# Kernel tuning notes

Measured on AMD Instinct MI355X. Metric: run time of the kernel, lower is better.

## Reference

```python
import jax, jax.numpy as jnp
import numpy as np

B, H, W, C = 4, 64, 64, 256
CQ = C // 8


def setup_inputs() -> dict:
    key = jax.random.key(0)
    ks = jax.random.split(key, 5)
    scale = 0.02
    inputs = jax.random.normal(ks[0], (B, H, W, C), dtype=jnp.float32)
    wq = jax.random.normal(ks[1], (C, CQ), dtype=jnp.float32) * scale
    bq = jnp.zeros((CQ,), dtype=jnp.float32)
    wk = jax.random.normal(ks[2], (C, CQ), dtype=jnp.float32) * scale
    bk = jnp.zeros((CQ,), dtype=jnp.float32)
    wv = jax.random.normal(ks[3], (C, C), dtype=jnp.float32) * scale
    bv = jnp.zeros((C,), dtype=jnp.float32)
    gamma = jax.random.normal(ks[4], (), dtype=jnp.float32)
    return {"inputs": inputs, "wq": wq, "bq": bq, "wk": wk, "bk": bk,
            "wv": wv, "bv": bv, "gamma": gamma}


def reference(inputs, wq, bq, wk, bk, wv, bv, gamma):
    b, h, w, c = inputs.shape
    n = h * w
    x = inputs.reshape(b, n, c)  # [B, N, C]
    # 1x1 convs == per-pixel linear projections
    q = x @ wq + bq              # [B, N, Cq]
    k = x @ wk + bk              # [B, N, Cq]
    v = x @ wv + bv              # [B, N, C]
    # energy = Q K^T (no sqrt scaling, as in the original)
    energy = jnp.einsum('bnd,bmd->bnm', q, k)      # [B, N, N]
    attention = jax.nn.softmax(energy, axis=-1)    # softmax over keys
    # x_out = V^T @ attention^T -> per query: sum_m attn[n,m] * v[m]
    x_out = jnp.einsum('bnm,bmc->bnc', attention, v)  # [B, N, C]
    x_out = x_out.reshape(b, h, w, c)
    return gamma * x_out + inputs
```

## Files before the change

kernel.cpp:

```cpp
#include <hip/hip_runtime.h>
#include <hip/hip_bf16.h>

typedef __attribute__((ext_vector_type(8))) short bf16x8;
typedef __attribute__((ext_vector_type(4))) float f32x4;
typedef __attribute__((ext_vector_type(16))) float f32x16;
typedef __attribute__((ext_vector_type(4))) int int4v;

#define NB 4
#define NN 4096
#define NC 256
#define NSPLIT 4
#define KEYS_PER_SPLIT 1024
#define KT_ITERS 16
#define LOG2E 1.4426950408889634f

__device__ __forceinline__ unsigned short f2bf(float f) {
    unsigned u = __builtin_bit_cast(unsigned, f);
    u += 0x7fffu + ((u >> 16) & 1u);
    return (unsigned short)(u >> 16);
}
__device__ __forceinline__ float bf2f(unsigned short u) {
    unsigned v = ((unsigned)u) << 16;
    return __builtin_bit_cast(float, v);
}
__device__ __forceinline__ void load_lds16(const void* g, void* l) {
    __builtin_amdgcn_global_load_lds(
        (const __attribute__((address_space(1))) void*)g,
        (__attribute__((address_space(3))) void*)l, 16, 0, 0);
}
__device__ __forceinline__ unsigned cvtpk(float lo, float hi) {
    unsigned d;
    asm("v_cvt_pk_bf16_f32 %0, %1, %2" : "=v"(d) : "v"(lo), "v"(hi));
    return d;
}
__device__ __forceinline__ void pl32swap(unsigned &a, unsigned &b) {
    asm volatile("v_permlane32_swap_b32 %0, %1" : "+v"(a), "+v"(b));
}
__device__ __forceinline__ float fexp2(float x) {
    float r;
    asm("v_exp_f32 %0, %1" : "=v"(r) : "v"(x));
    return r;
}

__global__ __launch_bounds__(256) void wt_kernel(
    const float* __restrict__ wq, const float* __restrict__ wk,
    const float* __restrict__ wv, unsigned short* __restrict__ wt)
{
    const int c = blockIdx.x;
    const int k = threadIdx.x;
    float v;
    if (c < 32)      v = wq[k * 32 + c];
    else if (c < 64) v = wk[k * 32 + (c - 32)] * LOG2E;
    else             v = wv[k * 256 + (c - 64)];
    wt[c * 256 + k] = f2bf(v);
}

__global__ __launch_bounds__(256) void proj_kernel(
    const float* __restrict__ x,
    const unsigned short* __restrict__ wt,
    const float* __restrict__ bq, const float* __restrict__ bk,
    const float* __restrict__ bv,
    unsigned short* __restrict__ q_ws,
    unsigned short* __restrict__ k_ws,
    unsigned short* __restrict__ vt_ws)
{
    const int lane = threadIdx.x & 63;
    const int w    = threadIdx.x >> 6;
    const int l15  = lane & 15, hh = lane >> 4;
    const int m0   = blockIdx.x * 16;
    const int ct0  = w * 5;

    f32x4 acc[5];
    #pragma unroll
    for (int i = 0; i < 5; ++i) acc[i] = f32x4{0.f, 0.f, 0.f, 0.f};

    const float* xrow = x + (size_t)(m0 + l15) * 256 + hh * 8;
    #pragma unroll
    for (int ks = 0; ks < 8; ++ks) {
        float4 xa = ((const float4*)(xrow + ks * 32))[0];
        float4 xb = ((const float4*)(xrow + ks * 32))[1];
        bf16x8 afrag;
        afrag[0] = (short)f2bf(xa.x); afrag[1] = (short)f2bf(xa.y);
        afrag[2] = (short)f2bf(xa.z); afrag[3] = (short)f2bf(xa.w);
        afrag[4] = (short)f2bf(xb.x); afrag[5] = (short)f2bf(xb.y);
        afrag[6] = (short)f2bf(xb.z); afrag[7] = (short)f2bf(xb.w);
        #pragma unroll
        for (int c = 0; c < 5; ++c) {
            bf16x8 bfrag = *(const bf16x8*)(wt + (size_t)((ct0 + c) * 16 + l15) * 256 + ks * 32 + hh * 8);
            acc[c] = __builtin_amdgcn_mfma_f32_16x16x32_bf16(afrag, bfrag, acc[c], 0, 0, 0);
        }
    }

    const int b    = m0 >> 12;
    const int nloc = m0 & 4095;
    #pragma unroll
    for (int c = 0; c < 5; ++c) {
        const int ct = ct0 + c;
        const int c0 = ct * 16;
        float bias;
        if (c0 < 32)      bias = bq[c0 + l15];
        else if (c0 < 64) bias = bk[c0 - 32 + l15] * LOG2E;
        else              bias = bv[c0 - 64 + l15];
        if (c0 < 64) {
            unsigned short* dst = (c0 < 32) ? q_ws : k_ws;
            const int cc = (c0 < 32) ? c0 : (c0 - 32);
            #pragma unroll
            for (int i = 0; i < 4; ++i)
                dst[(size_t)(m0 + hh * 4 + i) * 32 + cc + l15] = f2bf(acc[c][i] + bias);
        } else {
            const int cc = c0 - 64 + l15;
            #pragma unroll
            for (int i = 0; i < 4; i += 2) {
                unsigned lo = f2bf(acc[c][i]     + bias);
                unsigned hi = f2bf(acc[c][i + 1] + bias);
                *(unsigned*)(vt_ws + ((size_t)b * 256 + cc) * 4096 + nloc + hh * 4 + i)
                    = lo | (hi << 16);
            }
        }
    }
}

__global__ __launch_bounds__(256, 4) void attn_kernel(
    const unsigned short* __restrict__ q_ws,
    const unsigned short* __restrict__ k_ws,
    const unsigned short* __restrict__ vt_ws,
    unsigned short* __restrict__ opart,
    float* __restrict__ lpart)
{
    __shared__ unsigned short vt_lds[256 * 64];

    const int lane = threadIdx.x & 63;
    const int wid  = threadIdx.x >> 6;
    const int l31  = lane & 31;
    const int hi   = lane >> 5;
    const int wr   = wid >> 1;
    const int wc   = wid & 1;

    const int xcd   = blockIdx.x & 7;
    const int j     = blockIdx.x >> 3;
    const int combo = xcd * 2 + (j >> 6);
    const int qtile = j & 63;
    const int split = combo >> 2;
    const int b     = combo & 3;
    const int q0    = qtile * 64;
    const int key0  = split * KEYS_PER_SPLIT;

    bf16x8 aq[2];
    #pragma unroll
    for (int cs = 0; cs < 2; ++cs)
        aq[cs] = *(const bf16x8*)(q_ws +
            (size_t)(b * 4096 + q0 + wr * 32 + l31) * 32 + cs * 16 + hi * 8);

    f32x16 acc[4];
    #pragma unroll
    for (int ct = 0; ct < 4; ++ct)
        #pragma unroll
        for (int r = 0; r < 16; ++r) acc[ct][r] = 0.f;
    float lsum = 0.f;

    const unsigned short* vt_base = vt_ws + (size_t)b * 256 * 4096;
    const unsigned short* k_base  = k_ws + (size_t)b * 4096 * 32;

    for (int kt = 0; kt < KT_ITERS; ++kt) {
        const int kb = key0 + kt * 64;
        __syncthreads();

        #pragma unroll
        for (int e = 0; e < 8; ++e) {
            int idx  = e * 256 + threadIdx.x;
            int c    = idx >> 3;
            int slot = idx & 7;
            const unsigned short* src = vt_base + (size_t)c * 4096 + kb + ((slot ^ (c & 7)) << 3);
            load_lds16(src, (char*)vt_lds + idx * 16);
        }

        unsigned pa[4][4];
        #pragma unroll
        for (int ktile = 0; ktile < 2; ++ktile) {
            bf16x8 ak0 = *(const bf16x8*)(k_base +
                (size_t)(kb + ktile * 32 + l31) * 32 + hi * 8);
            bf16x8 ak1 = *(const bf16x8*)(k_base +
                (size_t)(kb + ktile * 32 + l31) * 32 + 16 + hi * 8);
            f32x16 e0;
            #pragma unroll
            for (int r = 0; r < 16; ++r) e0[r] = 0.f;
            e0 = __builtin_amdgcn_mfma_f32_32x32x16_bf16(ak0, aq[0], e0, 0, 0, 0);
            e0 = __builtin_amdgcn_mfma_f32_32x32x16_bf16(ak1, aq[1], e0, 0, 0, 0);

            float s = 0.f;
            #pragma unroll
            for (int h = 0; h < 2; ++h) {
                float p0 = fexp2(e0[h*8+0]), p1 = fexp2(e0[h*8+1]);
                float p2 = fexp2(e0[h*8+2]), p3 = fexp2(e0[h*8+3]);
                float p4 = fexp2(e0[h*8+4]), p5 = fexp2(e0[h*8+5]);
                float p6 = fexp2(e0[h*8+6]), p7 = fexp2(e0[h*8+7]);
                s += ((p0 + p1) + (p2 + p3)) + ((p4 + p5) + (p6 + p7));
                unsigned d0 = cvtpk(p0, p1);
                unsigned d1 = cvtpk(p2, p3);
                unsigned d2 = cvtpk(p4, p5);
                unsigned d3 = cvtpk(p6, p7);
                pl32swap(d0, d2);
                pl32swap(d1, d3);
                const int ks = ktile * 2 + h;
                pa[ks][0] = d0; pa[ks][1] = d1;
                pa[ks][2] = d2; pa[ks][3] = d3;
            }
            lsum += s;
        }
        __syncthreads();

        __builtin_amdgcn_s_setprio(1);
        #pragma unroll
        for (int ks = 0; ks < 4; ++ks) {
            union { unsigned u[4]; bf16x8 v; } cvt;
            cvt.u[0] = pa[ks][0]; cvt.u[1] = pa[ks][1];
            cvt.u[2] = pa[ks][2]; cvt.u[3] = pa[ks][3];
            #pragma unroll
            for (int ct = 0; ct < 4; ++ct) {
                int c = wc * 128 + ct * 32 + l31;
                int chunk = ks * 2 + hi;
                bf16x8 bvf = *(const bf16x8*)((char*)vt_lds + c * 128 + ((chunk ^ (c & 7)) << 4));
                acc[ct] = __builtin_amdgcn_mfma_f32_32x32x16_bf16(cvt.v, bvf, acc[ct], 0, 0, 0);
            }
        }
        __builtin_amdgcn_s_setprio(0);
    }

    lsum += __shfl_xor(lsum, 32);

    const size_t rowb = (size_t)(split * 4 + b) * 4096 + q0 + wr * 32;
    if (wc == 0 && hi == 0)
        lpart[rowb + l31] = lsum;

    #pragma unroll
    for (int ct = 0; ct < 4; ++ct) {
        int col = wc * 128 + ct * 32 + l31;
        #pragma unroll
        for (int rr = 0; rr < 16; ++rr) {
            int row = (rr & 3) + 8 * (rr >> 2) + 4 * hi;
            opart[(rowb + row) * 256 + col] = f2bf(acc[ct][rr]);
        }
    }
}

__global__ __launch_bounds__(256) void combine_kernel(
    const unsigned short* __restrict__ opart,
    const float* __restrict__ lpart,
    const float* __restrict__ x,
    const float* __restrict__ gamma_p,
    float* __restrict__ out)
{
    const int t  = blockIdx.x * 256 + threadIdx.x;
    const int r  = t >> 5;
    const int c0 = (t & 31) * 8;
    const float gamma = gamma_p[0];

    float sumO[8];
    #pragma unroll
    for (int j = 0; j < 8; ++j) sumO[j] = 0.f;
    float suml = 0.f;
    #pragma unroll
    for (int s = 0; s < NSPLIT; ++s) {
        bf16x8 o = *(const bf16x8*)(opart + ((size_t)(s * 16384 + r)) * 256 + c0);
        #pragma unroll
        for (int j = 0; j < 8; ++j) sumO[j] += bf2f((unsigned short)o[j]);
        suml += lpart[s * 16384 + r];
    }
    const float inv = gamma / suml;
    const size_t base = (size_t)r * 256 + c0;
    float4 x0 = *(const float4*)(x + base);
    float4 x1 = *(const float4*)(x + base + 4);
    float4 o0, o1;
    o0.x = sumO[0] * inv + x0.x; o0.y = sumO[1] * inv + x0.y;
    o0.z = sumO[2] * inv + x0.z; o0.w = sumO[3] * inv + x0.w;
    o1.x = sumO[4] * inv + x1.x; o1.y = sumO[5] * inv + x1.y;
    o1.z = sumO[6] * inv + x1.z; o1.w = sumO[7] * inv + x1.w;
    *(float4*)(out + base)     = o0;
    *(float4*)(out + base + 4) = o1;
}

extern "C" void kernel_launch(void* const* d_in, const int* in_sizes, int n_in,
                              void* d_out, int out_size, void* d_ws, size_t ws_size,
                              hipStream_t stream) {
    const float* x     = (const float*)d_in[0];
    const float* wq    = (const float*)d_in[1];
    const float* bq    = (const float*)d_in[2];
    const float* wk    = (const float*)d_in[3];
    const float* bk    = (const float*)d_in[4];
    const float* wv    = (const float*)d_in[5];
    const float* bv    = (const float*)d_in[6];
    const float* gamma = (const float*)d_in[7];
    float* out = (float*)d_out;

    char* ws = (char*)d_ws;
    unsigned short* wt    = (unsigned short*)(ws);
    unsigned short* q_ws  = (unsigned short*)(ws + 163840);
    unsigned short* k_ws  = (unsigned short*)(ws + 1212416);
    unsigned short* vt_ws = (unsigned short*)(ws + 2260992);
    unsigned short* opart = (unsigned short*)(ws + 10649600);
    float*          lpart = (float*)(ws + 44204032);

    wt_kernel     <<<320,  256, 0, stream>>>(wq, wk, wv, wt);
    proj_kernel   <<<1024, 256, 0, stream>>>(x, wt, bq, bk, bv, q_ws, k_ws, vt_ws);
    attn_kernel   <<<1024, 256, 0, stream>>>(q_ws, k_ws, vt_ws, opart, lpart);
    combine_kernel<<<2048, 256, 0, stream>>>(opart, lpart, x, gamma, out);
}
```

Before: 127.6 us.

## Double-buffer V tiles in LDS and double query tile per attention block

The attention kernel now runs 512-thread blocks covering 128 queries instead of 64, so each V tile staged in LDS feeds twice as many queries. A second LDS buffer lets the next V tile's asynchronous global-to-LDS load overlap with the QK^T, exp and PV MFMAs on the current tile. The swizzled LDS read addresses are now precomputed once per thread instead of on every read. The cost is 64KB of LDS per block, which limits how many blocks fit per CU, and half as many blocks in the grid.

Result: no change. 128.3 us (+0.6%).

```diff
diff --git a/kernel.cpp b/kernel.cpp
--- a/kernel.cpp
+++ b/kernel.cpp
@@ -120,14 +120,14 @@
     }
 }
 
-__global__ __launch_bounds__(256, 4) void attn_kernel(
+__global__ __launch_bounds__(512, 4) void attn_kernel(
     const unsigned short* __restrict__ q_ws,
     const unsigned short* __restrict__ k_ws,
     const unsigned short* __restrict__ vt_ws,
     unsigned short* __restrict__ opart,
     float* __restrict__ lpart)
 {
-    __shared__ unsigned short vt_lds[256 * 64];
+    __shared__ unsigned short vt_lds[2 * 256 * 64];
 
     const int lane = threadIdx.x & 63;
     const int wid  = threadIdx.x >> 6;
@@ -138,11 +138,11 @@
 
     const int xcd   = blockIdx.x & 7;
     const int j     = blockIdx.x >> 3;
-    const int combo = xcd * 2 + (j >> 6);
-    const int qtile = j & 63;
+    const int combo = xcd * 2 + (j >> 5);
+    const int qtile = j & 31;
     const int split = combo >> 2;
     const int b     = combo & 3;
-    const int q0    = qtile * 64;
+    const int q0    = qtile * 128;
     const int key0  = split * KEYS_PER_SPLIT;
 
     bf16x8 aq[2];
@@ -159,34 +159,40 @@
     float lsum = 0.f;
 
     const unsigned short* vt_base = vt_ws + (size_t)b * 256 * 4096;
-    const unsigned short* k_base  = k_ws + (size_t)b * 4096 * 32;
-
-    for (int kt = 0; kt < KT_ITERS; ++kt) {
-        const int kb = key0 + kt * 64;
-        __syncthreads();
-
-        #pragma unroll
-        for (int e = 0; e < 8; ++e) {
-            int idx  = e * 256 + threadIdx.x;
+    const unsigned short* kcur = k_ws + (size_t)b * 4096 * 32
+                               + (size_t)(key0 + l31) * 32 + hi * 8;
+
+    unsigned bvaddr[4];
+    #pragma unroll
+    for (int ct = 0; ct < 4; ++ct) {
+        int c = wc * 128 + ct * 32 + l31;
+        int x = c & 7;
+        bvaddr[ct] = (unsigned)(c * 128 + ((x & 6) << 4) + ((hi ^ (x & 1)) << 4));
+    }
+
+    unsigned pa[4][4];
+
+    auto STAGE = [&](int key, int lds_off) {
+        #pragma unroll
+        for (int e = 0; e < 4; ++e) {
+            int idx  = e * 512 + threadIdx.x;
             int c    = idx >> 3;
             int slot = idx & 7;
-            const unsigned short* src = vt_base + (size_t)c * 4096 + kb + ((slot ^ (c & 7)) << 3);
-            load_lds16(src, (char*)vt_lds + idx * 16);
-        }
-
-        unsigned pa[4][4];
+            const unsigned short* src = vt_base + (size_t)c * 4096 + key + ((slot ^ (c & 7)) << 3);
+            load_lds16(src, (char*)vt_lds + lds_off + idx * 16);
+        }
+    };
+
+    auto COMPUTEP = [&]() {
         #pragma unroll
         for (int ktile = 0; ktile < 2; ++ktile) {
-            bf16x8 ak0 = *(const bf16x8*)(k_base +
-                (size_t)(kb + ktile * 32 + l31) * 32 + hi * 8);
-            bf16x8 ak1 = *(const bf16x8*)(k_base +
-                (size_t)(kb + ktile * 32 + l31) * 32 + 16 + hi * 8);
+            bf16x8 ak0 = *(const bf16x8*)(kcur + ktile * 1024);
+            bf16x8 ak1 = *(const bf16x8*)(kcur + ktile * 1024 + 16);
             f32x16 e0;
             #pragma unroll
             for (int r = 0; r < 16; ++r) e0[r] = 0.f;
             e0 = __builtin_amdgcn_mfma_f32_32x32x16_bf16(ak0, aq[0], e0, 0, 0, 0);
             e0 = __builtin_amdgcn_mfma_f32_32x32x16_bf16(ak1, aq[1], e0, 0, 0, 0);
-
             float s = 0.f;
             #pragma unroll
             for (int h = 0; h < 2; ++h) {
@@ -207,8 +213,10 @@
             }
             lsum += s;
         }
-        __syncthreads();
-
+        kcur += 2048;
+    };
+
+    auto PV = [&](int lds_off) {
         __builtin_amdgcn_s_setprio(1);
         #pragma unroll
         for (int ks = 0; ks < 4; ++ks) {
@@ -217,13 +225,25 @@
             cvt.u[2] = pa[ks][2]; cvt.u[3] = pa[ks][3];
             #pragma unroll
             for (int ct = 0; ct < 4; ++ct) {
-                int c = wc * 128 + ct * 32 + l31;
-                int chunk = ks * 2 + hi;
-                bf16x8 bvf = *(const bf16x8*)((char*)vt_lds + c * 128 + ((chunk ^ (c & 7)) << 4));
+                bf16x8 bvf = *(const bf16x8*)((char*)vt_lds + lds_off + (bvaddr[ct] ^ (ks << 5)));
                 acc[ct] = __builtin_amdgcn_mfma_f32_32x32x16_bf16(cvt.v, bvf, acc[ct], 0, 0, 0);
             }
         }
         __builtin_amdgcn_s_setprio(0);
+    };
+
+    STAGE(key0, 0);
+
+    for (int kt2 = 0; kt2 < 8; ++kt2) {
+        const int kt = kt2 * 2;
+        __syncthreads();
+        STAGE(key0 + (kt + 1) * 64, 32768);
+        COMPUTEP();
+        PV(0);
+        __syncthreads();
+        if (kt2 != 7) STAGE(key0 + (kt + 2) * 64, 0);
+        COMPUTEP();
+        PV(32768);
     }
 
     lsum += __shfl_xor(lsum, 32);
@@ -302,6 +322,6 @@
 
     wt_kernel     <<<320,  256, 0, stream>>>(wq, wk, wv, wt);
     proj_kernel   <<<1024, 256, 0, stream>>>(x, wt, bq, bk, bv, q_ws, k_ws, vt_ws);
-    attn_kernel   <<<1024, 256, 0, stream>>>(q_ws, k_ws, vt_ws, opart, lpart);
+    attn_kernel   <<<512,  512, 0, stream>>>(q_ws, k_ws, vt_ws, opart, lpart);
     combine_kernel<<<2048, 256, 0, stream>>>(opart, lpart, x, gamma, out);
 }
```
